# Optimization experiments

Measured on AMD Instinct MI355X. Metric: run time of the kernel, lower is better.

The kernel has to match this reference:

```python
import jax, jax.numpy as jnp
import numpy as np

ORDER, IN_DIM, OUT_DIM, SEQ_LEN = 4096, 8, 1, 4096


def setup_inputs() -> dict:
    key = jax.random.key(0)
    ks = jax.random.split(key, 7)
    # reset_parameter uses uniform(-0.7, 0.7); A/C/L rescaled ~1/sqrt(order) for
    # numerical stability of the 4096-step linear recurrence (same math, stable values).
    sA = 0.9 * (3.0 / ORDER) ** 0.5
    sC = 0.7 / ORDER ** 0.5
    weight_a = jax.random.uniform(ks[0], (ORDER, ORDER), minval=-sA, maxval=sA, dtype=jnp.float32)
    weight_b = jax.random.uniform(ks[1], (ORDER, IN_DIM), minval=-0.7, maxval=0.7, dtype=jnp.float32)
    weight_c = jax.random.uniform(ks[2], (OUT_DIM, ORDER), minval=-sC, maxval=sC, dtype=jnp.float32)
    weight_d = jax.random.uniform(ks[3], (OUT_DIM, IN_DIM), minval=-0.7, maxval=0.7, dtype=jnp.float32)
    weight_l = jax.random.uniform(ks[4], (ORDER, 1), minval=-sC, maxval=sC, dtype=jnp.float32)
    u = jax.random.normal(ks[5], (IN_DIM, SEQ_LEN), dtype=jnp.float32)
    y_obs = jax.random.normal(ks[6], (1, SEQ_LEN), dtype=jnp.float32)
    return {"u": u, "y_obs": y_obs, "weight_a": weight_a, "weight_b": weight_b,
            "weight_c": weight_c, "weight_d": weight_d, "weight_l": weight_l}


def reference(u, y_obs, weight_a, weight_b, weight_c, weight_d, weight_l):
    # Observer (Luenberger) state-space recursion, inp_dim > 1 branch:
    #   y_t  = C h_t + D u_t
    #   h_{t+1} = A h_t + B u_t + L * (y_obs_t - y_t)
    # output = tanh(concat(y_t)) * 3, shape [out_dim, seq_len]
    order = weight_a.shape[0]
    h0 = jnp.ones((order, 1), dtype=u.dtype)  # nn.init.constant_(hidden, 1)

    def step(h, inp):
        u_t, yobs_t = inp  # u_t: [in_dim, 1], yobs_t: scalar
        y_t = weight_c @ h + weight_d @ u_t          # [out_dim, 1]
        h_next = weight_a @ h + weight_b @ u_t + weight_l * (yobs_t - y_t)
        return h_next, y_t

    u_seq = u.T[:, :, None]          # [seq_len, in_dim, 1]
    _, ys = jax.lax.scan(step, h0, (u_seq, y_obs[0]))
    y_hat = ys[:, :, 0].T            # [out_dim, seq_len]
    return jnp.tanh(y_hat) * 3
```

## Files before the change

kernel.cpp:

```cpp
#include <hip/hip_runtime.h>
#include <math.h>


constexpr int NDIM  = 4096;
constexpr int NC    = 10;
constexpr int SLAB  = 16 * 4096;
constexpr int JT    = 56;
constexpr int VAPPS = 28;
constexpr int KC    = NDIM / 32;
constexpr int TILES = NDIM / 16;

typedef float    f32x4  __attribute__((ext_vector_type(4)));
typedef _Float16 h16x8  __attribute__((ext_vector_type(8)));
typedef _Float16 f16;

__global__ __launch_bounds__(256) void k_build_a(
        const float* __restrict__ A, const float* __restrict__ C,
        const float* __restrict__ L, h16x8* __restrict__ AhSw) {
    __shared__ float lds[64][65];
    const int R0 = (blockIdx.x & 63) * 64;
    const int C0 = (blockIdx.x >> 6) * 64;
    const int tid = threadIdx.x;
    #pragma unroll
    for (int it = 0; it < 16; ++it) {
        const int r = it * 4 + (tid >> 6);
        const int c = tid & 63;
        lds[r][c] = A[(size_t)(R0 + r) * NDIM + C0 + c]
                  - L[R0 + r] * C[C0 + c];
    }
    __syncthreads();
    #pragma unroll
    for (int half = 0; half < 2; ++half) {
        const int o = half * 256 + tid;
        const int r = o >> 3;
        const int g = o & 7;
        union { h16x8 v; f16 h[8]; } pk;
        #pragma unroll
        for (int j = 0; j < 8; ++j) pk.h[j] = (f16)lds[r][g * 8 + j];
        const int tile = (R0 >> 4) + (r >> 4);
        const int kc   = (C0 >> 5) + (g >> 2);
        const int lane = (r & 15) | ((g & 3) << 4);
        AhSw[((size_t)tile * KC + kc) * 64 + lane] = pk.v;
    }
}

__global__ __launch_bounds__(256) void k_build_w0(
        const float* __restrict__ Bm, const float* __restrict__ Dm,
        const float* __restrict__ L,
        float* __restrict__ Wf, f16* __restrict__ Wh) {
    int k = blockIdx.x * blockDim.x + threadIdx.x;
    float Lk = L[k];
    float col[16];
    #pragma unroll
    for (int c = 0; c < 8; ++c) col[c] = Bm[k * 8 + c] - Lk * Dm[c];
    col[8] = Lk; col[9] = 1.0f;
    #pragma unroll
    for (int c = 10; c < 16; ++c) col[c] = 0.0f;
    #pragma unroll
    for (int c = 0; c < 16; ++c) {
        Wf[c * NDIM + k] = col[c];
        Wh[c * NDIM + k] = (f16)col[c];
    }
}

__global__ __launch_bounds__(256) void k_stepVR(
        const h16x8* __restrict__ AhSw, const f16* __restrict__ WhIn,
        float* __restrict__ WfOut, f16* __restrict__ WhOut,
        const float* __restrict__ Cvec,
        const float* __restrict__ RpartIn, float* __restrict__ RpartOut,
        float* __restrict__ gfSlot, const int r) {
    const int tid = threadIdx.x;

    if (blockIdx.x < 128) {
        __shared__ f32x4 red[4][64];
        const int lane = tid & 63, wave = tid >> 6;
        const int mr   = lane & 15, q = lane >> 4;
        const int tp   = blockIdx.x;
        const int tile = tp * 2 + (wave >> 1);
        const int kh   = wave & 1;
        const int k0   = kh * 2048;
        const bool liveB = (mr < NC);
        const h16x8* a8 = AhSw + ((size_t)tile * KC + kh * 64) * 64 + lane;
        const h16x8* b8 = (const h16x8*)WhIn + (((size_t)mr * NDIM + k0) >> 3) + q;

        f32x4 acc0 = {0,0,0,0}, acc1 = {0,0,0,0};
        for (int it = 0; it < 8; ++it) {
            h16x8 ra[8], rb[8];
            #pragma unroll
            for (int s = 0; s < 8; ++s) rb[s] = (h16x8){0,0,0,0,0,0,0,0};
            #pragma unroll
            for (int s = 0; s < 8; ++s) {
                const int c = it * 8 + s;
                ra[s] = a8[(size_t)c * 64];
            }
            if (liveB) {
                #pragma unroll
                for (int s = 0; s < 8; ++s) {
                    const int c = it * 8 + s;
                    rb[s] = b8[c * 4];
                }
            }
            #pragma unroll
            for (int s = 0; s < 8; ++s) {
                if (s & 1) acc1 = __builtin_amdgcn_mfma_f32_16x16x32_f16(ra[s], rb[s], acc1, 0, 0, 0);
                else       acc0 = __builtin_amdgcn_mfma_f32_16x16x32_f16(ra[s], rb[s], acc0, 0, 0, 0);
            }
        }
        red[wave][lane] = acc0 + acc1;
        __syncthreads();
        if (tid < 128) {
            const int half = tid >> 6;
            const int l    = tid & 63;
            f32x4 v = red[half * 2][l] + red[half * 2 + 1][l];
            const int col = l & 15;
            if (col < NC) {
                const int row0 = (tp * 2 + half) * 16;
                const int rb0  = row0 + ((l >> 4) << 2);
                #pragma unroll
                for (int i = 0; i < 4; ++i) {
                    WfOut[col * NDIM + rb0 + i] = v[i];
                    WhOut[col * NDIM + rb0 + i] = (f16)v[i];
                }
            }
        }
    } else {
        __shared__ float rp[4096];
        __shared__ float g8[8][33];
        __shared__ float gs[32];
        const int t = blockIdx.x - 128;

        if (r == 0) {
            if (tid < 32) gs[tid] = Cvec[t * 32 + tid];
        } else {
            #pragma unroll
            for (int i = 0; i < 16; ++i) {
                const int idx = tid + i * 256;
                rp[idx] = RpartIn[(size_t)(idx >> 5) * NDIM + t * 32 + (idx & 31)];
            }
            __syncthreads();
            {
                const int c = tid & 31, g = tid >> 5;
                float s = 0.0f;
                #pragma unroll
                for (int j = 0; j < 16; ++j) s += rp[(g * 16 + j) * 32 + c];
                g8[g][c] = s;
            }
            __syncthreads();
            if (tid < 32) {
                float s = 0.0f;
                #pragma unroll
                for (int g = 0; g < 8; ++g) s += g8[g][tid];
                gs[tid] = s;
            }
        }
        __syncthreads();
        if (tid < 32) gfSlot[t * 32 + tid] = gs[tid];

        if (r < VAPPS - 1) {
            float gl[32];
            #pragma unroll
            for (int j = 0; j < 32; ++j) gl[j] = gs[j];
            #pragma unroll
            for (int cc = 0; cc < 2; ++cc) {
                const int ch = tid * 2 + cc;
                float acc[8] = {};
                #pragma unroll
                for (int tt = 0; tt < 2; ++tt) {
                    const h16x8* fr = AhSw + (size_t)(t * 2 + tt) * (KC * 64)
                                    + (size_t)ch * 16;
                    #pragma unroll
                    for (int mrr = 0; mrr < 16; ++mrr) {
                        union { h16x8 v; f16 h[8]; } ua;
                        ua.v = fr[mrr];
                        const float gm = gl[tt * 16 + mrr];
                        #pragma unroll
                        for (int j = 0; j < 8; ++j) acc[j] += gm * (float)ua.h[j];
                    }
                }
                float4* op = (float4*)(RpartOut + (size_t)t * NDIM + 8 * ch);
                op[0] = make_float4(acc[0], acc[1], acc[2], acc[3]);
                op[1] = make_float4(acc[4], acc[5], acc[6], acc[7]);
            }
        }
    }
}

__global__ __launch_bounds__(256) void k_fbatch(
        const float* __restrict__ Wall, const float* __restrict__ C,
        const float* __restrict__ gf, float* __restrict__ F) {
    const int m = blockIdx.x;
    const float* W;
    const float* vec;
    if (m <= VAPPS) { W = Wall + (size_t)m * SLAB;     vec = C; }
    else            { W = Wall + (size_t)VAPPS * SLAB; vec = gf + (size_t)(m - VAPPS) * NDIM; }
    const int tid = threadIdx.x, lane = tid & 63, wave = tid >> 6;
    float acc[NC] = {};
    for (int k = tid; k < NDIM; k += 256) {
        float ck = vec[k];
        #pragma unroll
        for (int c = 0; c < NC; ++c) acc[c] += ck * W[c * NDIM + k];
    }
    __shared__ float red[4][NC];
    #pragma unroll
    for (int c = 0; c < NC; ++c) {
        float s = acc[c];
        #pragma unroll
        for (int off = 32; off > 0; off >>= 1) s += __shfl_down(s, off);
        if (lane == 0) red[wave][c] = s;
    }
    __syncthreads();
    if (tid < NC) F[m * NC + tid] = red[0][tid] + red[1][tid] + red[2][tid] + red[3][tid];
}

__global__ __launch_bounds__(256) void k_conv(
        const float* __restrict__ F, const float* __restrict__ u,
        const float* __restrict__ yobs, const float* __restrict__ Dm,
        float* __restrict__ out) {
    __shared__ float Fl[JT * NC];
    __shared__ float zw[(JT + 256) * 9];
    const int tid = threadIdx.x;
    const int t0  = blockIdx.x * 256;
    for (int idx = tid; idx < JT * NC; idx += 256) Fl[idx] = F[idx];
    for (int idx = tid; idx < (JT + 256) * 9; idx += 256) {
        int k = idx / 9, c = idx - k * 9;
        int s = t0 - JT + k;
        float v = 0.0f;
        if (s >= 0 && s < NDIM) v = (c < 8) ? u[c * NDIM + s] : yobs[s];
        zw[idx] = v;
    }
    __syncthreads();
    const int t = t0 + tid;
    float y = (t < JT) ? Fl[t * NC + 9] : 0.0f;
    #pragma unroll
    for (int c = 0; c < 8; ++c) y += Dm[c] * u[c * NDIM + t];
    for (int j = 0; j < JT; ++j) {
        const float* fj = Fl + j * NC;
        const float* zz = zw + (tid + JT - 1 - j) * 9;
        float p = 0.0f;
        #pragma unroll
        for (int c = 0; c < 9; ++c) p += fj[c] * zz[c];
        y += p;
    }
    out[t] = 3.0f * tanhf(y);
}

extern "C" void kernel_launch(void* const* d_in, const int* in_sizes, int n_in,
                              void* d_out, int out_size, void* d_ws, size_t ws_size,
                              hipStream_t stream) {
    const float* u    = (const float*)d_in[0];
    const float* yobs = (const float*)d_in[1];
    const float* A    = (const float*)d_in[2];
    const float* Bm   = (const float*)d_in[3];
    const float* C    = (const float*)d_in[4];
    const float* Dm   = (const float*)d_in[5];
    const float* L    = (const float*)d_in[6];
    float* out = (float*)d_out;

    char* ws = (char*)d_ws;
    h16x8* AhSw  = (h16x8*)ws;
    float* Wf    = (float*)(ws + 33554432ull);
    f16*   Wh    = (f16*)(ws + 41156608ull);
    float* gf    = (float*)(ws + 44957696ull);
    float* Rpart = (float*)(ws + 45416448ull);
    float* F     = (float*)(ws + 49610752ull);

    constexpr size_t RPN = (size_t)128 * NDIM;

    k_build_a<<<dim3(64 * 64), dim3(256), 0, stream>>>(A, C, L, AhSw);
    k_build_w0<<<dim3(16), dim3(256), 0, stream>>>(Bm, Dm, L, Wf, Wh);

    for (int r = 0; r < VAPPS; ++r) {
        const size_t in   = (size_t)r * SLAB;
        const size_t out_ = (size_t)(r + 1) * SLAB;
        const float* rin  = Rpart + ((r + 1) & 1) * RPN;
        float*       rout = Rpart + (r & 1) * RPN;
        k_stepVR<<<dim3(256), dim3(256), 0, stream>>>(
            AhSw, Wh + in, Wf + out_, Wh + out_,
            C, rin, rout, gf + (size_t)r * NDIM, r);
    }

    k_fbatch<<<dim3(JT), dim3(256), 0, stream>>>(Wf, C, gf, F);
    k_conv<<<dim3(16), dim3(256), 0, stream>>>(F, u, yobs, Dm, out);
}
```

Before: 462.3 us.

## Quantize A to per-row int8 for the transposed vector-product stage

Adds a per-row absmax pass and a new kernel that writes an int8 row-major copy of the fp16 A matrix along with per-row scales. The stage in each step kernel that multiplies the 32-element g slice by A rows now reads int8 rows with coalesced 16-byte loads instead of strided fp16 fragments from the swizzled layout. This halves the bytes read in that part of the step and improves coalescing, at the cost of an extra quantization pass and int8 rounding error in a 4096-step recurrence.

Result: faster. 438.8 us (-5.1%).

```diff
diff --git a/kernel.cpp b/kernel.cpp
--- a/kernel.cpp
+++ b/kernel.cpp
@@ -16,7 +16,8 @@
 
 __global__ __launch_bounds__(256) void k_build_a(
         const float* __restrict__ A, const float* __restrict__ C,
-        const float* __restrict__ L, h16x8* __restrict__ AhSw) {
+        const float* __restrict__ L, h16x8* __restrict__ AhSw,
+        unsigned int* __restrict__ rowmaxU) {
     __shared__ float lds[64][65];
     const int R0 = (blockIdx.x & 63) * 64;
     const int C0 = (blockIdx.x >> 6) * 64;
@@ -29,6 +30,12 @@
                   - L[R0 + r] * C[C0 + c];
     }
     __syncthreads();
+    if (tid < 64) {
+        float mx = 0.0f;
+        #pragma unroll 8
+        for (int c = 0; c < 64; ++c) mx = fmaxf(mx, fabsf(lds[tid][c]));
+        atomicMax(&rowmaxU[R0 + tid], __float_as_uint(mx));
+    }
     #pragma unroll
     for (int half = 0; half < 2; ++half) {
         const int o = half * 256 + tid;
@@ -44,11 +51,37 @@
     }
 }
 
+__global__ __launch_bounds__(256) void k_quant_r(
+        const h16x8* __restrict__ AhSw, const unsigned int* __restrict__ rowmaxU,
+        signed char* __restrict__ A8r, float* __restrict__ sAr) {
+    const size_t idx = (size_t)blockIdx.x * blockDim.x + threadIdx.x;
+    const int lane = (int)(idx & 63);
+    const int kc   = (int)((idx >> 6) & (KC - 1));
+    const int tile = (int)(idx >> 13);
+    const int row  = tile * 16 + (lane & 15);
+    const int col  = kc * 32 + (lane >> 4) * 8;
+    const float rm  = __uint_as_float(rowmaxU[row]);
+    const float inv = rm > 0.0f ? 127.0f / rm : 0.0f;
+    union { h16x8 v; f16 h[8]; } uh;
+    uh.v = AhSw[idx];
+    union { long l; signed char c[8]; } uo;
+    #pragma unroll
+    for (int j = 0; j < 8; ++j) {
+        int qv = (int)rintf((float)uh.h[j] * inv);
+        qv = qv > 127 ? 127 : (qv < -127 ? -127 : qv);
+        uo.c[j] = (signed char)qv;
+    }
+    *(long*)(A8r + (size_t)row * NDIM + col) = uo.l;
+    if (kc == 0 && (lane >> 4) == 0) sAr[row] = rm / 127.0f;
+}
+
 __global__ __launch_bounds__(256) void k_build_w0(
         const float* __restrict__ Bm, const float* __restrict__ Dm,
         const float* __restrict__ L,
-        float* __restrict__ Wf, f16* __restrict__ Wh) {
+        float* __restrict__ Wf, f16* __restrict__ Wh,
+        unsigned int* __restrict__ rowmaxU) {
     int k = blockIdx.x * blockDim.x + threadIdx.x;
+    rowmaxU[k] = 0u;
     float Lk = L[k];
     float col[16];
     #pragma unroll
@@ -64,7 +97,9 @@
 }
 
 __global__ __launch_bounds__(256) void k_stepVR(
-        const h16x8* __restrict__ AhSw, const f16* __restrict__ WhIn,
+        const h16x8* __restrict__ AhSw,
+        const signed char* __restrict__ A8r, const float* __restrict__ sAr,
+        const f16* __restrict__ WhIn,
         float* __restrict__ WfOut, f16* __restrict__ WhOut,
         const float* __restrict__ Cvec,
         const float* __restrict__ RpartIn, float* __restrict__ RpartOut,
@@ -80,7 +115,7 @@
         const int kh   = wave & 1;
         const int k0   = kh * 2048;
         const bool liveB = (mr < NC);
-        const h16x8* a8 = AhSw + ((size_t)tile * KC + kh * 64) * 64 + lane;
+        const h16x8* a8 = AhSw + ((size_t)tile * KC + (size_t)kh * 64) * 64 + lane;
         const h16x8* b8 = (const h16x8*)WhIn + (((size_t)mr * NDIM + k0) >> 3) + q;
 
         f32x4 acc0 = {0,0,0,0}, acc1 = {0,0,0,0};
@@ -159,28 +194,27 @@
         if (r < VAPPS - 1) {
             float gl[32];
             #pragma unroll
-            for (int j = 0; j < 32; ++j) gl[j] = gs[j];
-            #pragma unroll
-            for (int cc = 0; cc < 2; ++cc) {
-                const int ch = tid * 2 + cc;
-                float acc[8] = {};
-                #pragma unroll
-                for (int tt = 0; tt < 2; ++tt) {
-                    const h16x8* fr = AhSw + (size_t)(t * 2 + tt) * (KC * 64)
-                                    + (size_t)ch * 16;
-                    #pragma unroll
-                    for (int mrr = 0; mrr < 16; ++mrr) {
-                        union { h16x8 v; f16 h[8]; } ua;
-                        ua.v = fr[mrr];
-                        const float gm = gl[tt * 16 + mrr];
-                        #pragma unroll
-                        for (int j = 0; j < 8; ++j) acc[j] += gm * (float)ua.h[j];
-                    }
+            for (int j = 0; j < 32; ++j) gl[j] = gs[j] * sAr[t * 32 + j];
+            const int c0 = tid * 16;
+            float acc[16] = {};
+            const int4* arow = (const int4*)(A8r + (size_t)(t * 32) * NDIM + c0);
+            for (int rr = 0; rr < 32; ++rr) {
+                const int4 v = arow[(size_t)rr * (NDIM / 16)];
+                const float gm = gl[rr];
+                const int w0 = v.x, w1 = v.y, w2 = v.z, w3 = v.w;
+                #pragma unroll
+                for (int b = 0; b < 4; ++b) {
+                    acc[b]      += gm * (float)((w0 << (24 - 8 * b)) >> 24);
+                    acc[4 + b]  += gm * (float)((w1 << (24 - 8 * b)) >> 24);
+                    acc[8 + b]  += gm * (float)((w2 << (24 - 8 * b)) >> 24);
+                    acc[12 + b] += gm * (float)((w3 << (24 - 8 * b)) >> 24);
                 }
-                float4* op = (float4*)(RpartOut + (size_t)t * NDIM + 8 * ch);
-                op[0] = make_float4(acc[0], acc[1], acc[2], acc[3]);
-                op[1] = make_float4(acc[4], acc[5], acc[6], acc[7]);
-            }
+            }
+            float4* op = (float4*)(RpartOut + (size_t)t * NDIM + c0);
+            op[0] = make_float4(acc[0],  acc[1],  acc[2],  acc[3]);
+            op[1] = make_float4(acc[4],  acc[5],  acc[6],  acc[7]);
+            op[2] = make_float4(acc[8],  acc[9],  acc[10], acc[11]);
+            op[3] = make_float4(acc[12], acc[13], acc[14], acc[15]);
         }
     }
 }
@@ -257,17 +291,21 @@
     float* out = (float*)d_out;
 
     char* ws = (char*)d_ws;
-    h16x8* AhSw  = (h16x8*)ws;
-    float* Wf    = (float*)(ws + 33554432ull);
-    f16*   Wh    = (f16*)(ws + 41156608ull);
-    float* gf    = (float*)(ws + 44957696ull);
-    float* Rpart = (float*)(ws + 45416448ull);
-    float* F     = (float*)(ws + 49610752ull);
+    h16x8*        AhSw    = (h16x8*)ws;
+    signed char*  A8r     = (signed char*)(ws + 33554432ull);
+    float*        Wf      = (float*)(ws + 50331648ull);
+    f16*          Wh      = (f16*)(ws + 57933824ull);
+    float*        gf      = (float*)(ws + 61734912ull);
+    float*        Rpart   = (float*)(ws + 62193664ull);
+    float*        F       = (float*)(ws + 66387968ull);
+    float*        sAr     = (float*)(ws + 66390208ull);
+    unsigned int* rowmaxU = (unsigned int*)(ws + 66406592ull);
 
     constexpr size_t RPN = (size_t)128 * NDIM;
 
-    k_build_a<<<dim3(64 * 64), dim3(256), 0, stream>>>(A, C, L, AhSw);
-    k_build_w0<<<dim3(16), dim3(256), 0, stream>>>(Bm, Dm, L, Wf, Wh);
+    k_build_w0<<<dim3(16), dim3(256), 0, stream>>>(Bm, Dm, L, Wf, Wh, rowmaxU);
+    k_build_a<<<dim3(64 * 64), dim3(256), 0, stream>>>(A, C, L, AhSw, rowmaxU);
+    k_quant_r<<<dim3(TILES * KC * 64 / 256), dim3(256), 0, stream>>>(AhSw, rowmaxU, A8r, sAr);
 
     for (int r = 0; r < VAPPS; ++r) {
         const size_t in   = (size_t)r * SLAB;
@@ -275,7 +313,7 @@
         const float* rin  = Rpart + ((r + 1) & 1) * RPN;
         float*       rout = Rpart + (r & 1) * RPN;
         k_stepVR<<<dim3(256), dim3(256), 0, stream>>>(
-            AhSw, Wh + in, Wf + out_, Wh + out_,
+            AhSw, A8r, sAr, Wh + in, Wf + out_, Wh + out_,
             C, rin, rout, gf + (size_t)r * NDIM, r);
     }
 
```
